# Kernel optimization log

Hardware: AMD Instinct MI355X
Metric: run time of the kernel (lower is better)

The kernel has to match this reference:

```python
import jax, jax.numpy as jnp
import numpy as np

# Predictive-coding graph message passing (PCGraphConv core compute).
# Single-graph edge list (edge_src -> edge_dst) with one scalar weight per edge,
# tiled over the batch (weights.repeat(1, batchsize) in the original).
# PredictionMessagePassing: mu_i = sum_{e: dst(e)=i} w_e * f(x_{src(e)})
# ValueMessagePassing:      dx_j = -eps_j + f'(x_j) * sum_{e: src(e)=j} w_e * eps_{dst(e)}
# with eps = x - mu and f = tanh.

N_PER_GRAPH = 4096
E_PER_GRAPH = 524288
BATCH = 32


def setup_inputs() -> dict:
    key = jax.random.key(0)
    k1, k2, k3, k4 = jax.random.split(key, 4)
    x = jax.random.normal(k1, (BATCH * N_PER_GRAPH,), dtype=jnp.float32)
    weights = jax.random.normal(k2, (E_PER_GRAPH,), dtype=jnp.float32) * (1.0 / np.sqrt(N_PER_GRAPH))
    edge_src = jax.random.randint(k3, (E_PER_GRAPH,), 0, N_PER_GRAPH, dtype=jnp.int32)
    edge_dst = jax.random.randint(k4, (E_PER_GRAPH,), 0, N_PER_GRAPH, dtype=jnp.int32)
    return {"x": x, "weights": weights, "edge_src": edge_src, "edge_dst": edge_dst,
            "batch_size": BATCH, "num_vertices": N_PER_GRAPH}


def reference(x, weights, edge_src, edge_dst, batch_size, num_vertices):
    B, N = batch_size, num_vertices
    BN = B * N
    # Tile single-graph edges across the batch with per-graph node offsets.
    offs = (jnp.arange(B, dtype=edge_src.dtype) * N)[:, None]        # [B,1]
    src = (edge_src[None, :] + offs).reshape(-1)                     # [B*E]
    dst = (edge_dst[None, :] + offs).reshape(-1)                     # [B*E]
    w = jnp.tile(weights, B)                                         # [B*E]

    fx = jnp.tanh(x)                                                 # f(x)
    # Predictions: gather f(x) at src, weight per edge, scatter-add at dst.
    mu = jax.ops.segment_sum(w * fx[src], dst, num_segments=BN)      # [B*N]
    eps = x - mu                                                     # errors
    fprime = 1.0 - fx * fx                                           # f'(x)
    # Value update: backward flow of errors along edges.
    dx = -eps + fprime * jax.ops.segment_sum(w * eps[dst], src, num_segments=BN)
    return jnp.stack([mu, dx])                                       # [2, B*N]
```

## Files before the change

### kernel.cpp

```cpp
#include <hip/hip_runtime.h>


static constexpr int kB = 32, kLogB = 5;
static constexpr int kT = 8;
static constexpr int kNumBins = 512;
static constexpr int kChunkE = 2048;
static constexpr int kSlice = 20;
static constexpr int kStageCap = 1280;
static constexpr int kPad = 36;
static constexpr int kMaxRows = 256;

__device__ __forceinline__ unsigned short f2bf(float f) {
  unsigned u = __float_as_uint(f);
  u += 0x7fffu + ((u >> 16) & 1u);
  return (unsigned short)(u >> 16);
}
__device__ __forceinline__ float bf2f(unsigned h) {
  return __uint_as_float(h << 16);
}
__device__ __forceinline__ unsigned pack_rec(int other, int local, unsigned short wb) {
  return ((unsigned)other << 19) | ((unsigned)local << 16) | (unsigned)wb;
}

__global__ void __launch_bounds__(1024) k_binit(
    const float* __restrict__ x, const float* __restrict__ w,
    const int* __restrict__ esrc, const int* __restrict__ edst,
    float* __restrict__ x_t, float* __restrict__ fx_t,
    unsigned* __restrict__ binsA, unsigned* __restrict__ binsB,
    unsigned short* __restrict__ cntA, unsigned short* __restrict__ cntB,
    int N, int E, int nrows) {
  __shared__ int cA[kNumBins], cB[kNumBins];
  __shared__ float tile[32][65];
  int tid = threadIdx.x, blk = blockIdx.x;

  if (blk < nrows) {
    for (int t = tid; t < kNumBins; t += 1024) { cA[t] = 0; cB[t] = 0; }
    __syncthreads();
    int e0 = blk * kChunkE;
#pragma unroll
    for (int k = 0; k < kChunkE / 1024; k++) {
      int e = e0 + k * 1024 + tid;
      if (e < E) {
        int s = esrc[e], d = edst[e];
        unsigned short wb = f2bf(w[e]);
        int slotA = atomicAdd(&cA[d >> 3], 1);
        if (slotA < kSlice)
          binsA[((size_t)blk * kNumBins + (d >> 3)) * kSlice + slotA] =
              pack_rec(s, d & 7, wb);
        int slotB = atomicAdd(&cB[s >> 3], 1);
        if (slotB < kSlice)
          binsB[((size_t)blk * kNumBins + (s >> 3)) * kSlice + slotB] =
              pack_rec(d, s & 7, wb);
      }
    }
    __syncthreads();
    for (int t = tid; t < kNumBins; t += 1024) {
      cntA[(size_t)blk * kNumBins + t] = (unsigned short)min(cA[t], kSlice);
      cntB[(size_t)blk * kNumBins + t] = (unsigned short)min(cB[t], kSlice);
    }
  }

  if (blk < (N >> 6)) {
    int n0 = blk * 64;
    for (int k = tid; k < 32 * 64; k += 1024) {
      int b = k >> 6, n = k & 63;
      tile[b][n] = x[b * N + n0 + n];
    }
    __syncthreads();
    for (int k = tid; k < 64 * 32; k += 1024) {
      int n = k >> 5, b = k & 31;
      float xv = tile[b][n];
      int j = (n0 + n) * kB + b;
      x_t[j] = xv;
      fx_t[j] = tanhf(xv);
    }
  }
}

__global__ void __launch_bounds__(1024) k_accum(
    const unsigned* __restrict__ bins, const unsigned short* __restrict__ cnt,
    const float* __restrict__ vals, const float* __restrict__ x_t,
    const float* __restrict__ fx_t, float* __restrict__ eps_t,
    float* __restrict__ out, int N, int nrows, int mode) {
  __shared__ float rep[32 * kT * kPad];
  __shared__ unsigned stg[kStageCap];
  __shared__ int cntL[kMaxRows];
  __shared__ int scan[kMaxRows];
  int tid = threadIdx.x, t = blockIdx.x;
  int b = tid & 31, slot = tid >> 5;
  float* my = rep + slot * (kT * kPad);
#pragma unroll
  for (int l = 0; l < kT; l++) my[l * kPad + b] = 0.0f;

  if (tid < kMaxRows) {
    int c = (tid < nrows) ? (int)cnt[(size_t)tid * kNumBins + t] : 0;
    cntL[tid] = c;
    scan[tid] = c;
  }
  __syncthreads();
  for (int off = 1; off < kMaxRows; off <<= 1) {
    int v = 0;
    if (tid < kMaxRows && tid >= off) v = scan[tid - off];
    __syncthreads();
    if (tid < kMaxRows && tid >= off) scan[tid] += v;
    __syncthreads();
  }
  int T = min(scan[kMaxRows - 1], kStageCap);

  for (int r = slot; r < nrows; r += 32) {
    int c = cntL[r];
    int base = scan[r] - c;
    if (b < c) {
      int p = base + b;
      if (p < kStageCap)
        stg[p] = bins[((size_t)r * kNumBins + t) * kSlice + b];
    }
  }
  __syncthreads();

  int i = slot;
  unsigned r0 = (i      < T) ? stg[i]      : 0u;
  unsigned r1 = (i + 32 < T) ? stg[i + 32] : 0u;
  unsigned r2 = (i + 64 < T) ? stg[i + 64] : 0u;
  unsigned r3 = (i + 96 < T) ? stg[i + 96] : 0u;
  float v0 = (i      < T) ? vals[((r0 >> 19) << kLogB) + b] : 0.0f;
  float v1 = (i + 32 < T) ? vals[((r1 >> 19) << kLogB) + b] : 0.0f;
  float v2 = (i + 64 < T) ? vals[((r2 >> 19) << kLogB) + b] : 0.0f;
  while (i < T) {
    unsigned r4 = (i + 128 < T) ? stg[i + 128] : 0u;
    float v3 = (i + 96 < T) ? vals[((r3 >> 19) << kLogB) + b] : 0.0f;
    my[((r0 >> 16) & 7) * kPad + b] += bf2f(r0 & 0xffffu) * v0;
    r0 = r1; r1 = r2; r2 = r3; r3 = r4;
    v0 = v1; v1 = v2; v2 = v3;
    i += 32;
  }
  __syncthreads();

  if (tid < kT * kB) {
    int local = tid & 7, bb = tid >> 3;
    float s = 0.0f;
#pragma unroll
    for (int sl = 0; sl < 32; sl++) s += rep[sl * (kT * kPad) + local * kPad + bb];
    int n = t * kT + local;
    int j = n * kB + bb;
    if (mode == 0) {
      out[bb * N + n] = s;
      eps_t[j] = x_t[j] - s;
    } else {
      float fx = fx_t[j];
      out[bb * N + n] = fmaf(1.0f - fx * fx, s, -eps_t[j]);
    }
  }
}

extern "C" void kernel_launch(void* const* d_in, const int* in_sizes, int n_in,
                              void* d_out, int out_size, void* d_ws, size_t ws_size,
                              hipStream_t stream) {
  const float* x    = (const float*)d_in[0];
  const float* w    = (const float*)d_in[1];
  const int*   esrc = (const int*)d_in[2];
  const int*   edst = (const int*)d_in[3];

  int BN = in_sizes[0];
  int E  = in_sizes[1];
  int N  = BN / kB;
  int nrows = (E + kChunkE - 1) / kChunkE;

  float* ws    = (float*)d_ws;
  float* x_t   = ws;
  float* fx_t  = ws + (size_t)BN;
  float* eps_t = ws + 2 * (size_t)BN;
  unsigned short* cntA = (unsigned short*)(ws + 3 * (size_t)BN);
  unsigned short* cntB = cntA + (size_t)kMaxRows * kNumBins;
  unsigned* binsA = (unsigned*)(cntB + (size_t)kMaxRows * kNumBins);
  unsigned* binsB = binsA + (size_t)kMaxRows * kNumBins * kSlice;

  float* out_mu = (float*)d_out;
  float* out_dx = (float*)d_out + BN;

  int nblk1 = max(nrows, N >> 6);

  k_binit<<<nblk1, 1024, 0, stream>>>(x, w, esrc, edst, x_t, fx_t,
                                      binsA, binsB, cntA, cntB, N, E, nrows);
  k_accum<<<kNumBins, 1024, 0, stream>>>(binsA, cntA, fx_t, x_t, fx_t,
                                         eps_t, out_mu, N, nrows, 0);
  k_accum<<<kNumBins, 1024, 0, stream>>>(binsB, cntB, eps_t, x_t, fx_t,
                                         eps_t, out_dx, N, nrows, 1);
}
```

Measured before the change: 110.1 us.

## Replace capped per-chunk bins with full CSR built via histogram, scan, scatter

Builds exact per-node CSR adjacency for both edge directions using a shared-memory histogram, a block prefix scan, and an atomic scatter. Each pass then has warps gather along contiguous per-node edge lists with fp32 weights, replacing the capped bf16 bin records and the shared replicated accumulators. This removes the per-bin slot cap and the in-kernel staging scan. In exchange it adds kernel launches, a memset, and random global atomics during the scatter.

```diff
diff --git a/kernel.cpp b/kernel.cpp
--- a/kernel.cpp
+++ b/kernel.cpp
@@ -2,66 +2,37 @@
 
 
 static constexpr int kB = 32, kLogB = 5;
-static constexpr int kT = 8;
-static constexpr int kNumBins = 512;
-static constexpr int kChunkE = 2048;
-static constexpr int kSlice = 20;
-static constexpr int kStageCap = 1280;
-static constexpr int kPad = 36;
-static constexpr int kMaxRows = 256;
+static constexpr int kN = 4096;
+static constexpr int kHB = 128;
+static constexpr int kSB = 256;
 
-__device__ __forceinline__ unsigned short f2bf(float f) {
-  unsigned u = __float_as_uint(f);
-  u += 0x7fffu + ((u >> 16) & 1u);
-  return (unsigned short)(u >> 16);
-}
-__device__ __forceinline__ float bf2f(unsigned h) {
-  return __uint_as_float(h << 16);
-}
-__device__ __forceinline__ unsigned pack_rec(int other, int local, unsigned short wb) {
-  return ((unsigned)other << 19) | ((unsigned)local << 16) | (unsigned)wb;
-}
-
-__global__ void __launch_bounds__(1024) k_binit(
-    const float* __restrict__ x, const float* __restrict__ w,
-    const int* __restrict__ esrc, const int* __restrict__ edst,
+__global__ void __launch_bounds__(1024) k_prep(
+    const float* __restrict__ x, const int* __restrict__ esrc,
+    const int* __restrict__ edst,
     float* __restrict__ x_t, float* __restrict__ fx_t,
-    unsigned* __restrict__ binsA, unsigned* __restrict__ binsB,
-    unsigned short* __restrict__ cntA, unsigned short* __restrict__ cntB,
-    int N, int E, int nrows) {
-  __shared__ int cA[kNumBins], cB[kNumBins];
+    unsigned* __restrict__ g_cntA, unsigned* __restrict__ g_cntB,
+    int N, int E) {
+  __shared__ unsigned hA[kN], hB[kN];
   __shared__ float tile[32][65];
   int tid = threadIdx.x, blk = blockIdx.x;
 
-  if (blk < nrows) {
-    for (int t = tid; t < kNumBins; t += 1024) { cA[t] = 0; cB[t] = 0; }
+  if (blk < kHB) {
+    for (int t = tid; t < kN; t += 1024) { hA[t] = 0u; hB[t] = 0u; }
     __syncthreads();
-    int e0 = blk * kChunkE;
-#pragma unroll
-    for (int k = 0; k < kChunkE / 1024; k++) {
-      int e = e0 + k * 1024 + tid;
-      if (e < E) {
-        int s = esrc[e], d = edst[e];
-        unsigned short wb = f2bf(w[e]);
-        int slotA = atomicAdd(&cA[d >> 3], 1);
-        if (slotA < kSlice)
-          binsA[((size_t)blk * kNumBins + (d >> 3)) * kSlice + slotA] =
-              pack_rec(s, d & 7, wb);
-        int slotB = atomicAdd(&cB[s >> 3], 1);
-        if (slotB < kSlice)
-          binsB[((size_t)blk * kNumBins + (s >> 3)) * kSlice + slotB] =
-              pack_rec(d, s & 7, wb);
-      }
+    int chunk = (E + kHB - 1) / kHB;
+    int e0 = blk * chunk, e1 = min(e0 + chunk, E);
+    for (int e = e0 + tid; e < e1; e += 1024) {
+      atomicAdd(&hA[edst[e]], 1u);
+      atomicAdd(&hB[esrc[e]], 1u);
     }
     __syncthreads();
-    for (int t = tid; t < kNumBins; t += 1024) {
-      cntA[(size_t)blk * kNumBins + t] = (unsigned short)min(cA[t], kSlice);
-      cntB[(size_t)blk * kNumBins + t] = (unsigned short)min(cB[t], kSlice);
+    for (int t = tid; t < kN; t += 1024) {
+      unsigned a = hA[t], b = hB[t];
+      if (a) atomicAdd(&g_cntA[t], a);
+      if (b) atomicAdd(&g_cntB[t], b);
     }
-  }
-
-  if (blk < (N >> 6)) {
-    int n0 = blk * 64;
+  } else {
+    int n0 = (blk - kHB) * 64;
     for (int k = tid; k < 32 * 64; k += 1024) {
       int b = k >> 6, n = k & 63;
       tile[b][n] = x[b * N + n0 + n];
@@ -77,78 +48,91 @@
   }
 }
 
-__global__ void __launch_bounds__(1024) k_accum(
-    const unsigned* __restrict__ bins, const unsigned short* __restrict__ cnt,
+__global__ void __launch_bounds__(1024) k_scan(
+    const unsigned* __restrict__ g_cntA, const unsigned* __restrict__ g_cntB,
+    unsigned* __restrict__ g_offA, unsigned* __restrict__ g_offB) {
+  __shared__ unsigned ssum[1024];
+  const unsigned* cnt = blockIdx.x ? g_cntB : g_cntA;
+  unsigned* off = blockIdx.x ? g_offB : g_offA;
+  int tid = threadIdx.x;
+  uint4 c = reinterpret_cast<const uint4*>(cnt)[tid];
+  unsigned s = c.x + c.y + c.z + c.w;
+  ssum[tid] = s;
+  __syncthreads();
+  for (int o = 1; o < 1024; o <<= 1) {
+    unsigned v = 0;
+    if (tid >= o) v = ssum[tid - o];
+    __syncthreads();
+    if (tid >= o) ssum[tid] += v;
+    __syncthreads();
+  }
+  unsigned base = ssum[tid] - s;
+  uint4 o4;
+  o4.x = base;
+  o4.y = base + c.x;
+  o4.z = base + c.x + c.y;
+  o4.w = base + c.x + c.y + c.z;
+  reinterpret_cast<uint4*>(off)[tid] = o4;
+}
+
+__global__ void __launch_bounds__(1024) k_scatter(
+    const float* __restrict__ w, const int* __restrict__ esrc,
+    const int* __restrict__ edst,
+    unsigned* __restrict__ g_offA, unsigned* __restrict__ g_offB,
+    uint2* __restrict__ csrA, uint2* __restrict__ csrB, int E) {
+  int tid = blockIdx.x * 1024 + threadIdx.x;
+  int stride = gridDim.x * 1024;
+  for (int e = tid; e < E; e += stride) {
+    int s = esrc[e], d = edst[e];
+    unsigned wbits = __float_as_uint(w[e]);
+    unsigned a = atomicAdd(&g_offA[d], 1u);
+    csrA[a] = make_uint2((unsigned)s, wbits);
+    unsigned bsl = atomicAdd(&g_offB[s], 1u);
+    csrB[bsl] = make_uint2((unsigned)d, wbits);
+  }
+}
+
+__global__ void __launch_bounds__(256) k_pass(
+    const uint2* __restrict__ csr, const unsigned* __restrict__ off,
     const float* __restrict__ vals, const float* __restrict__ x_t,
     const float* __restrict__ fx_t, float* __restrict__ eps_t,
-    float* __restrict__ out, int N, int nrows, int mode) {
-  __shared__ float rep[32 * kT * kPad];
-  __shared__ unsigned stg[kStageCap];
-  __shared__ int cntL[kMaxRows];
-  __shared__ int scan[kMaxRows];
-  int tid = threadIdx.x, t = blockIdx.x;
-  int b = tid & 31, slot = tid >> 5;
-  float* my = rep + slot * (kT * kPad);
-#pragma unroll
-  for (int l = 0; l < kT; l++) my[l * kPad + b] = 0.0f;
+    float* __restrict__ out, int N, int mode) {
+  __shared__ float red[256];
+  int tid = threadIdx.x;
+  int b = tid & 31, hw = tid >> 5;
+  int nl = hw >> 2, part = hw & 3;
+  int n = blockIdx.x * 2 + nl;
+  int lo = n ? (int)off[n - 1] : 0;
+  int T = (int)off[n];
 
-  if (tid < kMaxRows) {
-    int c = (tid < nrows) ? (int)cnt[(size_t)tid * kNumBins + t] : 0;
-    cntL[tid] = c;
-    scan[tid] = c;
+  float acc = 0.0f;
+  int i = lo + part;
+  uint2 z = make_uint2(0u, 0u);
+  uint2 r0 = (i < T) ? csr[i] : z;
+  uint2 r1 = (i + 4 < T) ? csr[i + 4] : z;
+  uint2 r2 = (i + 8 < T) ? csr[i + 8] : z;
+  float v0 = (i < T) ? vals[(r0.x << kLogB) + b] : 0.0f;
+  float v1 = (i + 4 < T) ? vals[(r1.x << kLogB) + b] : 0.0f;
+  while (i < T) {
+    uint2 r3 = (i + 12 < T) ? csr[i + 12] : z;
+    float v2 = (i + 8 < T) ? vals[(r2.x << kLogB) + b] : 0.0f;
+    acc = fmaf(__uint_as_float(r0.y), v0, acc);
+    r0 = r1; r1 = r2; r2 = r3;
+    v0 = v1; v1 = v2;
+    i += 4;
   }
-  __syncthreads();
-  for (int off = 1; off < kMaxRows; off <<= 1) {
-    int v = 0;
-    if (tid < kMaxRows && tid >= off) v = scan[tid - off];
-    __syncthreads();
-    if (tid < kMaxRows && tid >= off) scan[tid] += v;
-    __syncthreads();
-  }
-  int T = min(scan[kMaxRows - 1], kStageCap);
-
-  for (int r = slot; r < nrows; r += 32) {
-    int c = cntL[r];
-    int base = scan[r] - c;
-    if (b < c) {
-      int p = base + b;
-      if (p < kStageCap)
-        stg[p] = bins[((size_t)r * kNumBins + t) * kSlice + b];
-    }
-  }
+  red[tid] = acc;
   __syncthreads();
 
-  int i = slot;
-  unsigned r0 = (i      < T) ? stg[i]      : 0u;
-  unsigned r1 = (i + 32 < T) ? stg[i + 32] : 0u;
-  unsigned r2 = (i + 64 < T) ? stg[i + 64] : 0u;
-  unsigned r3 = (i + 96 < T) ? stg[i + 96] : 0u;
-  float v0 = (i      < T) ? vals[((r0 >> 19) << kLogB) + b] : 0.0f;
-  float v1 = (i + 32 < T) ? vals[((r1 >> 19) << kLogB) + b] : 0.0f;
-  float v2 = (i + 64 < T) ? vals[((r2 >> 19) << kLogB) + b] : 0.0f;
-  while (i < T) {
-    unsigned r4 = (i + 128 < T) ? stg[i + 128] : 0u;
-    float v3 = (i + 96 < T) ? vals[((r3 >> 19) << kLogB) + b] : 0.0f;
-    my[((r0 >> 16) & 7) * kPad + b] += bf2f(r0 & 0xffffu) * v0;
-    r0 = r1; r1 = r2; r2 = r3; r3 = r4;
-    v0 = v1; v1 = v2; v2 = v3;
-    i += 32;
-  }
-  __syncthreads();
-
-  if (tid < kT * kB) {
-    int local = tid & 7, bb = tid >> 3;
-    float s = 0.0f;
-#pragma unroll
-    for (int sl = 0; sl < 32; sl++) s += rep[sl * (kT * kPad) + local * kPad + bb];
-    int n = t * kT + local;
-    int j = n * kB + bb;
+  if (part == 0) {
+    float s = red[tid] + red[tid + 32] + red[tid + 64] + red[tid + 96];
+    int j = n * kB + b;
     if (mode == 0) {
-      out[bb * N + n] = s;
+      out[b * N + n] = s;
       eps_t[j] = x_t[j] - s;
     } else {
       float fx = fx_t[j];
-      out[bb * N + n] = fmaf(1.0f - fx * fx, s, -eps_t[j]);
+      out[b * N + n] = fmaf(1.0f - fx * fx, s, -eps_t[j]);
     }
   }
 }
@@ -164,26 +148,30 @@
   int BN = in_sizes[0];
   int E  = in_sizes[1];
   int N  = BN / kB;
-  int nrows = (E + kChunkE - 1) / kChunkE;
 
   float* ws    = (float*)d_ws;
   float* x_t   = ws;
   float* fx_t  = ws + (size_t)BN;
   float* eps_t = ws + 2 * (size_t)BN;
-  unsigned short* cntA = (unsigned short*)(ws + 3 * (size_t)BN);
-  unsigned short* cntB = cntA + (size_t)kMaxRows * kNumBins;
-  unsigned* binsA = (unsigned*)(cntB + (size_t)kMaxRows * kNumBins);
-  unsigned* binsB = binsA + (size_t)kMaxRows * kNumBins * kSlice;
+  unsigned* g_cntA = (unsigned*)(ws + 3 * (size_t)BN);
+  unsigned* g_cntB = g_cntA + N;
+  unsigned* g_offA = g_cntB + N;
+  unsigned* g_offB = g_offA + N;
+  uint2* csrA = (uint2*)(g_offB + N);
+  uint2* csrB = csrA + (size_t)E;
 
   float* out_mu = (float*)d_out;
   float* out_dx = (float*)d_out + BN;
 
-  int nblk1 = max(nrows, N >> 6);
+  hipMemsetAsync(g_cntA, 0, (size_t)2 * N * sizeof(unsigned), stream);
 
-  k_binit<<<nblk1, 1024, 0, stream>>>(x, w, esrc, edst, x_t, fx_t,
-                                      binsA, binsB, cntA, cntB, N, E, nrows);
-  k_accum<<<kNumBins, 1024, 0, stream>>>(binsA, cntA, fx_t, x_t, fx_t,
-                                         eps_t, out_mu, N, nrows, 0);
-  k_accum<<<kNumBins, 1024, 0, stream>>>(binsB, cntB, eps_t, x_t, fx_t,
-                                         eps_t, out_dx, N, nrows, 1);
+  k_prep<<<kHB + (N >> 6), 1024, 0, stream>>>(x, esrc, edst, x_t, fx_t,
+                                              g_cntA, g_cntB, N, E);
+  k_scan<<<2, 1024, 0, stream>>>(g_cntA, g_cntB, g_offA, g_offB);
+  k_scatter<<<kSB, 1024, 0, stream>>>(w, esrc, edst, g_offA, g_offB,
+                                      csrA, csrB, E);
+  k_pass<<<N / 2, 256, 0, stream>>>(csrA, g_offA, fx_t, x_t, fx_t,
+                                    eps_t, out_mu, N, 0);
+  k_pass<<<N / 2, 256, 0, stream>>>(csrB, g_offB, eps_t, x_t, fx_t,
+                                    eps_t, out_dx, N, 1);
 }
```

Result: slower. 172.2 us (+56.4%).
